# Performance work log

Measured on AMD Instinct MI355X. Metric: run time of the kernel, lower is better.

The kernel has to match this reference:

```python
import jax, jax.numpy as jnp
import numpy as np

EPS = 1e-5

def _conv3x3(x, w):
    # x: [n,c,h,w], w: [o,c,3,3], stride 1, padding 1 (SAME)
    return jax.lax.conv_general_dilated(x, w, (1, 1), 'SAME',
                                        dimension_numbers=('NCHW', 'OIHW', 'NCHW'))

def _bn(x, g, b, m, v):
    # inference-mode BatchNorm2d with running stats
    s = g / jnp.sqrt(v + EPS)
    return x * s[:, None, None] + (b - m * s)[:, None, None]

def _lrelu(x):
    return jnp.where(x > 0, x, 0.2 * x)

def _conv1x1(x, w, b):
    # w: [o,c] (1x1 conv kernel collapsed)
    return jnp.einsum('nchw,oc->nohw', x, w) + b[:, None, None]

def _conv_relu(x, w, g, b, m, v):
    return _lrelu(_bn(_conv3x3(x, w), g, b, m, v))

def _pam(f, Wq, bq, Wk, bk, Wv, bv, alpha):
    n, c, h, w = f.shape
    hw = h * w
    q = _conv1x1(f, Wq, bq).reshape(n, -1, hw)   # [n,cr,hw]
    k = _conv1x1(f, Wk, bk).reshape(n, -1, hw)   # [n,cr,hw]
    # attention[i,j] over spatial tokens, softmax along j
    attn = jax.nn.softmax(jnp.einsum('nci,ncj->nij', q, k), axis=-1)  # [n,hw,hw]
    v = _conv1x1(f, Wv, bv).reshape(n, c, hw)    # [n,c,hw]
    # torch: bmm(v, attn^T) -> out[:, :, i] = sum_j v[:, :, j] * attn[i, j]
    out = jnp.einsum('ncj,nij->nci', v, attn).reshape(n, c, h, w)
    return alpha * out + f

def _cam(f, W1, b1, W2, b2):
    s = jnp.mean(f, axis=(2, 3), keepdims=True)  # AdaptiveAvgPool2d(1)
    s = _lrelu(_conv1x1(s, W1, b1))
    s = jax.nn.sigmoid(_conv1x1(s, W2, b2))
    return f * s

def _upx2(x):
    n, c, h, w = x.shape
    return jax.image.resize(x, (n, c, 2 * h, 2 * w), 'bilinear')

def setup_inputs() -> dict:
    key = jax.random.key(0)
    ks = jax.random.split(key, 16)
    N, C, H, W_ = 4, 512, 64, 64
    CR, NC = C // 8, 64
    f32 = jnp.float32
    def nrm(k, shape, s=0.05):
        return jax.random.normal(k, shape, f32) * s
    return {
        'x': jax.random.normal(ks[0], (N, C, H, W_), f32),
        'W_pam_in': nrm(ks[1], (C, C, 3, 3)),
        'pam_gamma': jnp.ones((C,), f32), 'pam_beta': jnp.zeros((C,), f32),
        'pam_mean': nrm(ks[2], (C,)), 'pam_var': jax.random.uniform(ks[3], (C,), f32) + 0.5,
        'Wq': nrm(ks[4], (CR, C)), 'bq': jnp.zeros((CR,), f32),
        'Wk': nrm(ks[5], (CR, C)), 'bk': jnp.zeros((CR,), f32),
        'Wv': nrm(ks[6], (C, C)), 'bv': jnp.zeros((C,), f32),
        'alpha': nrm(ks[7], (1,), 1.0),
        'W_pam_out': nrm(ks[8], (NC, C)), 'b_pam_out': jnp.zeros((NC,), f32),
        'W_cam_in': nrm(ks[9], (C, C, 3, 3)),
        'cam_gamma': jnp.ones((C,), f32), 'cam_beta': jnp.zeros((C,), f32),
        'cam_mean': nrm(ks[10], (C,)), 'cam_var': jax.random.uniform(ks[11], (C,), f32) + 0.5,
        'Wc1': nrm(ks[12], (CR, C)), 'bc1': jnp.zeros((CR,), f32),
        'Wc2': nrm(ks[13], (C, CR)), 'bc2': jnp.zeros((C,), f32),
        'W_cam_out': nrm(ks[14], (NC, C)), 'b_cam_out': jnp.zeros((NC,), f32),
    }

def reference(x, W_pam_in, pam_gamma, pam_beta, pam_mean, pam_var,
              Wq, bq, Wk, bk, Wv, bv, alpha, W_pam_out, b_pam_out,
              W_cam_in, cam_gamma, cam_beta, cam_mean, cam_var,
              Wc1, bc1, Wc2, bc2, W_cam_out, b_cam_out):
    pam_feat = _conv_relu(x, W_pam_in, pam_gamma, pam_beta, pam_mean, pam_var)
    pam_feat = _pam(pam_feat, Wq, bq, Wk, bk, Wv, bv, alpha)
    pam_feat = _upx2(_conv1x1(pam_feat, W_pam_out, b_pam_out))
    cam_feat = _conv_relu(x, W_cam_in, cam_gamma, cam_beta, cam_mean, cam_var)
    cam_feat = _cam(cam_feat, Wc1, bc1, Wc2, bc2)
    cam_feat = _upx2(_conv1x1(cam_feat, W_cam_out, b_cam_out))
    return pam_feat + cam_feat
```

## Files before the change

### kernel.cpp

```cpp
#include <hip/hip_runtime.h>
#include <hip/hip_bf16.h>
#include <math.h>

#define N_  4
#define C_  512
#define H_  64
#define W_  64
#define HW_ 4096
#define CR_ 64
#define NC_ 64
#define EPSV 1e-5f

typedef __attribute__((ext_vector_type(8))) __bf16 bf16x8;
typedef __attribute__((ext_vector_type(4))) float f32x4;
typedef __hip_bfloat16 bf16s;

__device__ __forceinline__ unsigned short bfb(float f) {
    union { bf16s h; unsigned short u; } cv;
    cv.h = __float2bfloat16(f);
    return cv.u;
}

__device__ __forceinline__ float b2f(unsigned short h) {
    union { unsigned u; float f; } c; c.u = ((unsigned)h) << 16; return c.f;
}

__device__ __forceinline__ int swz8(int row, int ch) {
    return row * 64 + ((ch ^ (row & 7)) << 3);
}

__global__ __launch_bounds__(256) void k_xpose(
    const float* __restrict__ x, bf16s* __restrict__ xbT)
{
    __shared__ float xs[64][65];
    const int tid = threadIdx.x;
    const int n = blockIdx.z, c0 = blockIdx.y * 64, p0 = blockIdx.x * 64;
    for (int e = tid; e < 4096; e += 256) {
        int ci = e >> 6, pi = e & 63;
        xs[ci][pi] = x[((size_t)(n*C_ + c0 + ci))*HW_ + p0 + pi];
    }
    __syncthreads();
    for (int e = tid; e < 4096; e += 256) {
        int pi = e >> 6, ci = e & 63;
        xbT[((size_t)n*HW_ + p0 + pi)*C_ + c0 + ci] = __float2bfloat16(xs[ci][pi]);
    }
}

__global__ __launch_bounds__(256) void k_wprep(
    const float* __restrict__ w, bf16s* __restrict__ wb)
{
    int e = blockIdx.x * 256 + threadIdx.x;
    int c = e & 511; int r = e >> 9;
    int tap = r % 9; int o = r / 9;
    wb[e] = __float2bfloat16(w[((size_t)o*C_ + c)*9 + tap]);
}

__global__ __launch_bounds__(256) void k_wcast(
    const float* __restrict__ in, bf16s* __restrict__ out, int nElem)
{
    int e = blockIdx.x * 256 + threadIdx.x;
    if (e < nElem) out[e] = __float2bfloat16(in[e]);
}

__global__ __launch_bounds__(256, 3) void k_conv3x3_mfma(
    const bf16s* __restrict__ xbT,
    const bf16s* __restrict__ wb,  const bf16s* __restrict__ wb2,
    const float* __restrict__ gamma,  const float* __restrict__ beta,
    const float* __restrict__ mean,   const float* __restrict__ var,
    const float* __restrict__ gamma2, const float* __restrict__ beta2,
    const float* __restrict__ mean2,  const float* __restrict__ var2,
    bf16s* __restrict__ featT, bf16s* __restrict__ featT2,
    float* __restrict__ csum)
{
    __shared__ bf16s aL[3][128][36];
    __shared__ bf16s bL[132][36];
    const int tid = threadIdx.x;
    const int lid = blockIdx.x + (blockIdx.y << 5) + (blockIdx.z << 8);
    const int xcd = lid & 7;
    const int half = xcd >> 2;
    const int n    = xcd & 3;
    const int w8   = lid >> 3;
    const int o0 = (w8 >> 5) * 128;
    const int pt = w8 & 31;
    const int y0 = pt * 2;
    const bf16s* wbs = half ? wb2 : wb;
    const float* gm = half ? gamma2 : gamma;
    const float* bt = half ? beta2  : beta;
    const float* mn = half ? mean2  : mean;
    const float* vr = half ? var2   : var;
    bf16s* ft = half ? featT2 : featT;
    const int lane = tid & 63;
    const int wid  = tid >> 6;
    const int wr = wid >> 1, wc = wid & 1;
    const int lr = lane & 15, cb = lane >> 4;

    const int ao  = tid >> 2;
    const int ac  = (tid & 3) * 8;
    const int t0  = tid >> 2;
    const int t1  = t0 + 64;
    const int t2  = t0 + 128;
    const int ry1 = t1 >= 66 ? 1 : 0;
    const int xi1 = t1 - (ry1 ? 66 : 0);

    f32x4 acc[4][4];
#pragma unroll
    for (int i = 0; i < 4; ++i)
#pragma unroll
        for (int j = 0; j < 4; ++j) acc[i][j] = (f32x4){0.f,0.f,0.f,0.f};

    int4 pA0, pA1, pA2, pA3, pA4, pA5, pB0, pB1, pB2;

#define CONV_AADDR(DXI, OHALF, C0, DYI) \
    (const int4*)(wbs + ((size_t)(o0 + (OHALF) + ao)*9 + (DYI)*3 + (DXI))*C_ + (C0) + ac)

#define CONV_BLOAD(DST, RY, XI, C0, DYI, VALID)                               \
    {                                                                         \
        int row_ = y0 + (DYI) - 1 + (RY);                                     \
        int xc_  = (XI) - 1;                                                  \
        int4 v_ = {0,0,0,0};                                                  \
        if ((VALID) && row_ >= 0 && row_ < H_ && xc_ >= 0 && xc_ < W_)        \
            v_ = *(const int4*)(xbT +                                         \
                ((size_t)n*HW_ + row_*W_ + xc_)*C_ + (C0) + ac);              \
        DST = v_;                                                             \
    }

#define CONV_ISSUE(C0, DYI)                                                   \
    {                                                                         \
        pA0 = *CONV_AADDR(0,  0, C0, DYI);                                    \
        pA1 = *CONV_AADDR(0, 64, C0, DYI);                                    \
        pA2 = *CONV_AADDR(1,  0, C0, DYI);                                    \
        pA3 = *CONV_AADDR(1, 64, C0, DYI);                                    \
        pA4 = *CONV_AADDR(2,  0, C0, DYI);                                    \
        pA5 = *CONV_AADDR(2, 64, C0, DYI);                                    \
        CONV_BLOAD(pB0, 0, t0, C0, DYI, 1)                                    \
        CONV_BLOAD(pB1, ry1, xi1, C0, DYI, 1)                                 \
        CONV_BLOAD(pB2, 1, t2 - 66, C0, DYI, tid < 16)                        \
    }

    CONV_ISSUE(0, 0)
    int c0 = 0, dyi = 0;
    for (int it = 0; it < 48; ++it) {
        *(int4*)&aL[0][ao][ac]      = pA0;
        *(int4*)&aL[0][64 + ao][ac] = pA1;
        *(int4*)&aL[1][ao][ac]      = pA2;
        *(int4*)&aL[1][64 + ao][ac] = pA3;
        *(int4*)&aL[2][ao][ac]      = pA4;
        *(int4*)&aL[2][64 + ao][ac] = pA5;
        *(int4*)&bL[t0][ac] = pB0;
        *(int4*)&bL[t1][ac] = pB1;
        if (tid < 16) *(int4*)&bL[t2][ac] = pB2;
        __syncthreads();
        int nd = dyi + 1, nc = c0;
        if (nd == 3) { nd = 0; nc += 32; }
        if (it < 47) CONV_ISSUE(nc, nd)
#pragma unroll
        for (int dxi = 0; dxi < 3; ++dxi) {
            bf16x8 af[4], bfv[4];
#pragma unroll
            for (int fm = 0; fm < 4; ++fm)
                af[fm] = *(const bf16x8*)&aL[dxi][wr*64 + fm*16 + lr][cb*8];
#pragma unroll
            for (int fn = 0; fn < 4; ++fn) {
                int pg = wc*64 + fn*16 + lr;
                int ry = pg >> 6, xc = pg & 63;
                bfv[fn] = *(const bf16x8*)&bL[ry*66 + xc + dxi][cb*8];
            }
#pragma unroll
            for (int fm = 0; fm < 4; ++fm)
#pragma unroll
                for (int fn = 0; fn < 4; ++fn)
                    acc[fm][fn] = __builtin_amdgcn_mfma_f32_16x16x32_bf16(
                        af[fm], bfv[fn], acc[fm][fn], 0, 0, 0);
        }
        __syncthreads();
        c0 = nc; dyi = nd;
    }
#undef CONV_ISSUE
#undef CONV_BLOAD
#undef CONV_AADDR
#pragma unroll
    for (int fm = 0; fm < 4; ++fm) {
        float sc[4], sh[4];
        const int obase = o0 + wr*64 + fm*16 + cb*4;
#pragma unroll
        for (int r = 0; r < 4; ++r) {
            int o = obase + r;
            sc[r] = gm[o] * rsqrtf(vr[o] + EPSV);
            sh[r] = bt[o] - mn[o]*sc[r];
        }
        float ps[4] = {0.f, 0.f, 0.f, 0.f};
#pragma unroll
        for (int fn = 0; fn < 4; ++fn) {
            int pg = wc*64 + fn*16 + lr;
            int p  = pt*128 + pg;
            float vv[4];
#pragma unroll
            for (int r = 0; r < 4; ++r) {
                float t = fmaf(acc[fm][fn][r], sc[r], sh[r]);
                vv[r] = t > 0.f ? t : 0.2f*t;
                ps[r] += vv[r];
            }
            uint2 u;
            u.x = (unsigned)bfb(vv[0]) | ((unsigned)bfb(vv[1]) << 16);
            u.y = (unsigned)bfb(vv[2]) | ((unsigned)bfb(vv[3]) << 16);
            *(uint2*)&ft[((size_t)n*HW_ + p)*C_ + obase] = u;
        }
        if (half) {
#pragma unroll
            for (int r = 0; r < 4; ++r) {
                float s = ps[r];
                s += __shfl_xor(s, 1);
                s += __shfl_xor(s, 2);
                s += __shfl_xor(s, 4);
                s += __shfl_xor(s, 8);
                if (lr == 0) atomicAdd(&csum[n*C_ + obase + r], s);
            }
        }
    }
}

__global__ __launch_bounds__(256, 2) void k_gemm_qkv(
    const bf16s* __restrict__ Wqk, const bf16s* __restrict__ Wv,
    const bf16s* __restrict__ Bt,
    const float* __restrict__ bq, const float* __restrict__ bk,
    const float* __restrict__ bv,
    bf16s* __restrict__ qkb, bf16s* __restrict__ vb)
{
    __shared__ bf16s aL[64][36];
    __shared__ bf16s bL[256][36];
    const int tid = threadIdx.x;
    const int flat = blockIdx.x + (blockIdx.y << 4) + blockIdx.z * 160;
    const int k8 = flat & 7;
    const int n  = k8 >> 1;
    const int xh = k8 & 1;
    const int w8 = flat >> 3;
    const int yy = w8 % 10;
    const int p0 = ((((w8 / 10) << 1) | xh)) << 8;
    const bool isqk = (yy < 2);
    const int o0 = isqk ? yy*64 : (yy - 2)*64;
    const bf16s* A = isqk ? Wqk : Wv;
    const int lane = tid & 63;
    const int wid  = tid >> 6;
    const int lr = lane & 15, cb = lane >> 4;
    const int arow = tid >> 2, ach = (tid & 3) * 8;

    f32x4 acc[4][4];
#pragma unroll
    for (int i = 0; i < 4; ++i)
#pragma unroll
        for (int j = 0; j < 4; ++j) acc[i][j] = (f32x4){0.f,0.f,0.f,0.f};

    int4 pA, pB0, pB1, pB2, pB3;

#define GEMM_ISSUE(C0)                                                        \
    {                                                                         \
        pA = *(const int4*)&A[(size_t)(o0 + arow)*C_ + (C0) + ach];           \
        pB0 = *(const int4*)&Bt[((size_t)n*HW_ + p0 + arow      )*C_ + (C0) + ach]; \
        pB1 = *(const int4*)&Bt[((size_t)n*HW_ + p0 + arow +  64)*C_ + (C0) + ach]; \
        pB2 = *(const int4*)&Bt[((size_t)n*HW_ + p0 + arow + 128)*C_ + (C0) + ach]; \
        pB3 = *(const int4*)&Bt[((size_t)n*HW_ + p0 + arow + 192)*C_ + (C0) + ach]; \
    }

    GEMM_ISSUE(0)
    for (int c0 = 0; c0 < C_; c0 += 32) {
        *(int4*)&aL[arow][ach] = pA;
        *(int4*)&bL[arow      ][ach] = pB0;
        *(int4*)&bL[arow +  64][ach] = pB1;
        *(int4*)&bL[arow + 128][ach] = pB2;
        *(int4*)&bL[arow + 192][ach] = pB3;
        __syncthreads();
        if (c0 + 32 < C_) GEMM_ISSUE(c0 + 32)
        bf16x8 af[4], bfv[4];
#pragma unroll
        for (int fo = 0; fo < 4; ++fo)
            af[fo] = *(const bf16x8*)&aL[fo*16 + lr][cb*8];
#pragma unroll
        for (int fp = 0; fp < 4; ++fp)
            bfv[fp] = *(const bf16x8*)&bL[wid*64 + fp*16 + lr][cb*8];
#pragma unroll
        for (int fo = 0; fo < 4; ++fo)
#pragma unroll
            for (int fp = 0; fp < 4; ++fp)
                acc[fo][fp] = __builtin_amdgcn_mfma_f32_16x16x32_bf16(
                    af[fo], bfv[fp], acc[fo][fp], 0, 0, 0);
        __syncthreads();
    }
#undef GEMM_ISSUE
#pragma unroll
    for (int fo = 0; fo < 4; ++fo) {
        const int obase = o0 + fo*16 + cb*4;
        const float* bp = isqk ? ((obase >> 6) ? bk : bq) : bv;
        const int bofs = isqk ? (obase & 63) : obase;
        float bv4[4];
#pragma unroll
        for (int r = 0; r < 4; ++r) bv4[r] = bp[bofs + r];
#pragma unroll
        for (int fp = 0; fp < 4; ++fp) {
            int p = p0 + wid*64 + fp*16 + lr;
            float v[4];
#pragma unroll
            for (int r = 0; r < 4; ++r) v[r] = acc[fo][fp][r] + bv4[r];
            if (isqk) {
                uint2 u;
                u.x = (unsigned)bfb(v[0]) | ((unsigned)bfb(v[1]) << 16);
                u.y = (unsigned)bfb(v[2]) | ((unsigned)bfb(v[3]) << 16);
                size_t base = (((size_t)((obase >> 6) * N_ + n))*HW_ + p)*64
                              + (obase & 63);
                *(uint2*)&qkb[base] = u;
            } else {
#pragma unroll
                for (int r = 0; r < 4; ++r)
                    vb[((size_t)(n*C_ + obase + r))*HW_ + p] =
                        __float2bfloat16(v[r]);
            }
        }
    }
}

__global__ __launch_bounds__(256, 2) void k_gemm(
    const bf16s* __restrict__ A, const bf16s* __restrict__ Bt,
    const float* __restrict__ bias, const float* __restrict__ scale,
    float* __restrict__ outp, int O)
{
    __shared__ bf16s aL[64][36];
    __shared__ bf16s bL[256][36];
    const int tid = threadIdx.x;
    const int n  = blockIdx.z;
    const int p0 = blockIdx.x * 256;
    const int o0 = blockIdx.y * 64;
    const int lane = tid & 63;
    const int wid  = tid >> 6;
    const int lr = lane & 15, cb = lane >> 4;
    const int arow = tid >> 2, ach = (tid & 3) * 8;

    f32x4 acc[4][4];
#pragma unroll
    for (int i = 0; i < 4; ++i)
#pragma unroll
        for (int j = 0; j < 4; ++j) acc[i][j] = (f32x4){0.f,0.f,0.f,0.f};

    int4 pA, pB0, pB1, pB2, pB3;
    float4 pS0, pS1;

#define GEMM_ISSUE(C0)                                                        \
    {                                                                         \
        pA = *(const int4*)&A[(size_t)(o0 + arow)*C_ + (C0) + ach];           \
        if (scale) {                                                          \
            pS0 = *(const float4*)&scale[(size_t)n*C_ + (C0) + ach];          \
            pS1 = *(const float4*)&scale[(size_t)n*C_ + (C0) + ach + 4];      \
        }                                                                     \
        pB0 = *(const int4*)&Bt[((size_t)n*HW_ + p0 + arow      )*C_ + (C0) + ach]; \
        pB1 = *(const int4*)&Bt[((size_t)n*HW_ + p0 + arow +  64)*C_ + (C0) + ach]; \
        pB2 = *(const int4*)&Bt[((size_t)n*HW_ + p0 + arow + 128)*C_ + (C0) + ach]; \
        pB3 = *(const int4*)&Bt[((size_t)n*HW_ + p0 + arow + 192)*C_ + (C0) + ach]; \
    }

    GEMM_ISSUE(0)
    for (int c0 = 0; c0 < C_; c0 += 32) {
        if (scale) {
            const bf16s* sp = (const bf16s*)&pA;
            bf16s tmp[8];
            tmp[0] = __float2bfloat16(__bfloat162float(sp[0]) * pS0.x);
            tmp[1] = __float2bfloat16(__bfloat162float(sp[1]) * pS0.y);
            tmp[2] = __float2bfloat16(__bfloat162float(sp[2]) * pS0.z);
            tmp[3] = __float2bfloat16(__bfloat162float(sp[3]) * pS0.w);
            tmp[4] = __float2bfloat16(__bfloat162float(sp[4]) * pS1.x);
            tmp[5] = __float2bfloat16(__bfloat162float(sp[5]) * pS1.y);
            tmp[6] = __float2bfloat16(__bfloat162float(sp[6]) * pS1.z);
            tmp[7] = __float2bfloat16(__bfloat162float(sp[7]) * pS1.w);
            *(int4*)&aL[arow][ach] = *(int4*)tmp;
        } else {
            *(int4*)&aL[arow][ach] = pA;
        }
        *(int4*)&bL[arow      ][ach] = pB0;
        *(int4*)&bL[arow +  64][ach] = pB1;
        *(int4*)&bL[arow + 128][ach] = pB2;
        *(int4*)&bL[arow + 192][ach] = pB3;
        __syncthreads();
        if (c0 + 32 < C_) GEMM_ISSUE(c0 + 32)
        bf16x8 af[4], bfv[4];
#pragma unroll
        for (int fo = 0; fo < 4; ++fo)
            af[fo] = *(const bf16x8*)&aL[fo*16 + lr][cb*8];
#pragma unroll
        for (int fp = 0; fp < 4; ++fp)
            bfv[fp] = *(const bf16x8*)&bL[wid*64 + fp*16 + lr][cb*8];
#pragma unroll
        for (int fo = 0; fo < 4; ++fo)
#pragma unroll
            for (int fp = 0; fp < 4; ++fp)
                acc[fo][fp] = __builtin_amdgcn_mfma_f32_16x16x32_bf16(
                    af[fo], bfv[fp], acc[fo][fp], 0, 0, 0);
        __syncthreads();
    }
#undef GEMM_ISSUE
#pragma unroll
    for (int fo = 0; fo < 4; ++fo) {
        const int obase = o0 + fo*16 + cb*4;
        float bv[4];
#pragma unroll
        for (int r = 0; r < 4; ++r) bv[r] = bias[obase + r];
#pragma unroll
        for (int fp = 0; fp < 4; ++fp) {
            int p = p0 + wid*64 + fp*16 + lr;
#pragma unroll
            for (int r = 0; r < 4; ++r)
                outp[((size_t)(n*O + obase + r))*HW_ + p] =
                    acc[fo][fp][r] + bv[r];
        }
    }
}

__global__ __launch_bounds__(256) void k_rowstats_mfma(
    const bf16s* __restrict__ qb, const bf16s* __restrict__ kb,
    float* __restrict__ rowm, float* __restrict__ rowl)
{
    __shared__ bf16s qs[4096];
    __shared__ bf16s ks[2][4096];
    const int tid = threadIdx.x;
    const int lid = blockIdx.x + (blockIdx.y << 6) + (blockIdx.z << 8);
    const int n  = lid & 3;
    const int jz = (lid >> 2) & 1;
    const int i0 = (lid >> 3) << 6;
    const int lane = tid & 63;
    const int wid  = tid >> 6;
    const int lr = lane & 15, cb = lane >> 4;

    for (int e = tid; e < 512; e += 256) {
        int row = e >> 3, ch = e & 7;
        *(int4*)&qs[swz8(row, ch)] =
            *(const int4*)&qb[((size_t)n*HW_ + i0 + row)*CR_ + ch*8];
    }
    const int krow = tid >> 3, kch = tid & 7;
    const bf16s* kbase = kb + (size_t)n*HW_*CR_ + (size_t)jz*2048*CR_ + kch*8;
    int4 kreg0 = *(const int4*)(kbase + (size_t)krow*CR_);
    int4 kreg1 = *(const int4*)(kbase + (size_t)(krow + 32)*CR_);
    *(int4*)&ks[0][swz8(krow, kch)] = kreg0;
    *(int4*)&ks[0][swz8(krow + 32, kch)] = kreg1;
    kreg0 = *(const int4*)(kbase + (size_t)(64 + krow)*CR_);
    kreg1 = *(const int4*)(kbase + (size_t)(64 + krow + 32)*CR_);
    __syncthreads();
    bf16x8 bq[2];
#pragma unroll
    for (int kk = 0; kk < 2; ++kk)
        bq[kk] = *(const bf16x8*)&qs[swz8(wid*16 + lr, kk*4 + cb)];

    float m_t = -INFINITY, l_t = 0.f;
    for (int t = 0; t < 32; ++t) {
        const bf16s* kst = ks[t & 1];
        f32x4 sv[4];
#pragma unroll
        for (int fj = 0; fj < 4; ++fj) {
            f32x4 s = (f32x4){0.f,0.f,0.f,0.f};
#pragma unroll
            for (int kk = 0; kk < 2; ++kk) {
                bf16x8 ak = *(const bf16x8*)&kst[swz8(fj*16 + lr, kk*4 + cb)];
                s = __builtin_amdgcn_mfma_f32_16x16x32_bf16(ak, bq[kk], s, 0, 0, 0);
            }
            sv[fj] = s;
        }
        if (t < 31) {
            *(int4*)&ks[(t + 1) & 1][swz8(krow, kch)] = kreg0;
            *(int4*)&ks[(t + 1) & 1][swz8(krow + 32, kch)] = kreg1;
            if (t < 30) {
                kreg0 = *(const int4*)(kbase + (size_t)((t+2)*64 + krow)*CR_);
                kreg1 = *(const int4*)(kbase + (size_t)((t+2)*64 + krow + 32)*CR_);
            }
        }
        float mx = m_t;
#pragma unroll
        for (int fj = 0; fj < 4; ++fj)
#pragma unroll
            for (int r = 0; r < 4; ++r) mx = fmaxf(mx, sv[fj][r]);
        float sum = 0.f;
#pragma unroll
        for (int fj = 0; fj < 4; ++fj)
#pragma unroll
            for (int r = 0; r < 4; ++r) sum += __expf(sv[fj][r] - mx);
        l_t = l_t * __expf(m_t - mx) + sum;
        m_t = mx;
        __syncthreads();
    }
#pragma unroll
    for (int mask = 16; mask <= 32; mask <<= 1) {
        float mo = __shfl_xor(m_t, mask);
        float lo = __shfl_xor(l_t, mask);
        float m2 = fmaxf(m_t, mo);
        l_t = l_t * __expf(m_t - m2) + lo * __expf(mo - m2);
        m_t = m2;
    }
    if (cb == 0) {
        rowm[((size_t)jz*N_ + n)*HW_ + i0 + wid*16 + lr] = m_t;
        rowl[((size_t)jz*N_ + n)*HW_ + i0 + wid*16 + lr] = l_t;
    }
}

__global__ __launch_bounds__(256, 4) void k_pv_mfma(
    const bf16s* __restrict__ qb, const bf16s* __restrict__ kb,
    const bf16s* __restrict__ vb, const float* __restrict__ rowm,
    const float* __restrict__ rowl, const float* __restrict__ alpha,
    bf16s* __restrict__ featT)
{
    __shared__ bf16s ks[2][4096];
    __shared__ bf16s ps[2][4096];
    const int tid = threadIdx.x;
    const int lid = blockIdx.x + (blockIdx.y << 6) + (blockIdx.z << 8);
    const int k8  = lid & 7;
    const int n   = k8 >> 1;
    const int cc0 = (((lid >> 3) & 1) * 2 + (k8 & 1)) << 7;
    const int i0  = (lid >> 4) << 6;
    const int lane = tid & 63;
    const int wid  = tid >> 6;
    const int lr = lane & 15, cb = lane >> 4;

    for (int e = tid; e < 512; e += 256) {
        int row = e >> 3, ch = e & 7;
        *(int4*)&ks[0][swz8(row, ch)] =
            *(const int4*)&qb[((size_t)n*HW_ + i0 + row)*CR_ + ch*8];
    }
    const int krow = tid >> 3, kch = tid & 7;
    const bf16s* kbase = kb + (size_t)n*HW_*CR_ + kch*8;
    int4 kreg0 = *(const int4*)(kbase + (size_t)krow*CR_);
    int4 kreg1 = *(const int4*)(kbase + (size_t)(krow + 32)*CR_);
    __syncthreads();
    bf16x8 bq[2];
#pragma unroll
    for (int kk = 0; kk < 2; ++kk)
        bq[kk] = *(const bf16x8*)&ks[0][swz8(wid*16 + lr, kk*4 + cb)];

    const size_t sidx = (size_t)n*HW_ + i0 + wid*16 + lr;
    const float m0 = rowm[sidx], m1 = rowm[sidx + (size_t)N_*HW_];
    const float l0 = rowl[sidx], l1 = rowl[sidx + (size_t)N_*HW_];
    const float mreg = fmaxf(m0, m1);
    const float rinv = 1.f / (l0*__expf(m0 - mreg) + l1*__expf(m1 - mreg));
    const float al = alpha[0];
    __syncthreads();
    *(int4*)&ks[0][swz8(krow, kch)] = kreg0;
    *(int4*)&ks[0][swz8(krow + 32, kch)] = kreg1;
    kreg0 = *(const int4*)(kbase + (size_t)(64 + krow)*CR_);
    kreg1 = *(const int4*)(kbase + (size_t)(64 + krow + 32)*CR_);
    __syncthreads();

    f32x4 acc[2][4];
#pragma unroll
    for (int i = 0; i < 2; ++i)
#pragma unroll
        for (int j = 0; j < 4; ++j) acc[i][j] = (f32x4){0.f,0.f,0.f,0.f};

    const bf16s* vbase = vb + ((size_t)(n*C_ + cc0 + wid*32))*HW_;
    bf16x8 vc0, vc1, vc2, vc3, vn0, vn1, vn2, vn3;

    for (int jt = 0; jt < 64; ++jt) {
        const bf16s* vj = vbase + jt*64;
        vn0 = *(const bf16x8*)(vj + (size_t)(     lr)*HW_      + cb*8);
        vn1 = *(const bf16x8*)(vj + (size_t)(16 + lr)*HW_      + cb*8);
        vn2 = *(const bf16x8*)(vj + (size_t)(     lr)*HW_ + 32 + cb*8);
        vn3 = *(const bf16x8*)(vj + (size_t)(16 + lr)*HW_ + 32 + cb*8);
        if (jt > 0) {
            const bf16s* pp = ps[(jt - 1) & 1];
            bf16x8 pa[4];
#pragma unroll
            for (int fi = 0; fi < 4; ++fi)
                pa[fi] = *(const bf16x8*)&pp[swz8(fi*16 + lr, cb)];
#pragma unroll
            for (int fi = 0; fi < 4; ++fi) {
                acc[0][fi] = __builtin_amdgcn_mfma_f32_16x16x32_bf16(
                    vc0, pa[fi], acc[0][fi], 0, 0, 0);
                acc[1][fi] = __builtin_amdgcn_mfma_f32_16x16x32_bf16(
                    vc1, pa[fi], acc[1][fi], 0, 0, 0);
            }
#pragma unroll
            for (int fi = 0; fi < 4; ++fi)
                pa[fi] = *(const bf16x8*)&pp[swz8(fi*16 + lr, 4 + cb)];
#pragma unroll
            for (int fi = 0; fi < 4; ++fi) {
                acc[0][fi] = __builtin_amdgcn_mfma_f32_16x16x32_bf16(
                    vc2, pa[fi], acc[0][fi], 0, 0, 0);
                acc[1][fi] = __builtin_amdgcn_mfma_f32_16x16x32_bf16(
                    vc3, pa[fi], acc[1][fi], 0, 0, 0);
            }
        }
        {
            const bf16s* kst = ks[jt & 1];
            bf16s* pst = ps[jt & 1];
#pragma unroll
            for (int fj = 0; fj < 4; ++fj) {
                f32x4 s = (f32x4){0.f,0.f,0.f,0.f};
#pragma unroll
                for (int kk = 0; kk < 2; ++kk) {
                    bf16x8 ak = *(const bf16x8*)&kst[swz8(fj*16 + lr, kk*4 + cb)];
                    s = __builtin_amdgcn_mfma_f32_16x16x32_bf16(ak, bq[kk], s, 0, 0, 0);
                }
                unsigned short b[4];
#pragma unroll
                for (int r = 0; r < 4; ++r)
                    b[r] = bfb(__expf(s[r] - mreg) * rinv);
                uint2 u;
                u.x = (unsigned)b[0] | ((unsigned)b[1] << 16);
                u.y = (unsigned)b[2] | ((unsigned)b[3] << 16);
                *(uint2*)&pst[swz8(wid*16 + lr, fj*2 + (cb >> 1)) + (cb & 1)*4] = u;
            }
        }
        if (jt < 63) {
            *(int4*)&ks[(jt + 1) & 1][swz8(krow, kch)] = kreg0;
            *(int4*)&ks[(jt + 1) & 1][swz8(krow + 32, kch)] = kreg1;
            if (jt < 62) {
                kreg0 = *(const int4*)(kbase + (size_t)((jt+2)*64 + krow)*CR_);
                kreg1 = *(const int4*)(kbase + (size_t)((jt+2)*64 + krow + 32)*CR_);
            }
        }
        vc0 = vn0; vc1 = vn1; vc2 = vn2; vc3 = vn3;
        __syncthreads();
    }
    {
        const bf16s* pp = ps[63 & 1];
        bf16x8 pa[4];
#pragma unroll
        for (int fi = 0; fi < 4; ++fi)
            pa[fi] = *(const bf16x8*)&pp[swz8(fi*16 + lr, cb)];
#pragma unroll
        for (int fi = 0; fi < 4; ++fi) {
            acc[0][fi] = __builtin_amdgcn_mfma_f32_16x16x32_bf16(
                vc0, pa[fi], acc[0][fi], 0, 0, 0);
            acc[1][fi] = __builtin_amdgcn_mfma_f32_16x16x32_bf16(
                vc1, pa[fi], acc[1][fi], 0, 0, 0);
        }
#pragma unroll
        for (int fi = 0; fi < 4; ++fi)
            pa[fi] = *(const bf16x8*)&pp[swz8(fi*16 + lr, 4 + cb)];
#pragma unroll
        for (int fi = 0; fi < 4; ++fi) {
            acc[0][fi] = __builtin_amdgcn_mfma_f32_16x16x32_bf16(
                vc2, pa[fi], acc[0][fi], 0, 0, 0);
            acc[1][fi] = __builtin_amdgcn_mfma_f32_16x16x32_bf16(
                vc3, pa[fi], acc[1][fi], 0, 0, 0);
        }
    }
#pragma unroll
    for (int fc2 = 0; fc2 < 2; ++fc2) {
        const int ccl = wid*32 + fc2*16 + cb*4;
#pragma unroll
        for (int fi = 0; fi < 4; ++fi) {
            const int p = i0 + fi*16 + lr;
            bf16s* fb = &featT[((size_t)n*HW_ + p)*C_ + cc0 + ccl];
            uint2 fv = *(const uint2*)fb;
            float f0 = b2f((unsigned short)(fv.x & 0xffff));
            float f1 = b2f((unsigned short)(fv.x >> 16));
            float f2 = b2f((unsigned short)(fv.y & 0xffff));
            float f3 = b2f((unsigned short)(fv.y >> 16));
            float v0 = fmaf(al, acc[fc2][fi][0], f0);
            float v1 = fmaf(al, acc[fc2][fi][1], f1);
            float v2 = fmaf(al, acc[fc2][fi][2], f2);
            float v3 = fmaf(al, acc[fc2][fi][3], f3);
            uint2 u;
            u.x = (unsigned)bfb(v0) | ((unsigned)bfb(v1) << 16);
            u.y = (unsigned)bfb(v2) | ((unsigned)bfb(v3) << 16);
            *(uint2*)fb = u;
        }
    }
}

__global__ __launch_bounds__(64) void k_cmlp(
    const float* __restrict__ s0, const float* __restrict__ Wc1,
    const float* __restrict__ bc1, const float* __restrict__ Wc2,
    const float* __restrict__ bc2, float* __restrict__ s2)
{
    const int n = blockIdx.x, tid = threadIdx.x;
    __shared__ float s1s[64];
    float a = 0.f;
    for (int c = 0; c < C_; ++c)
        a = fmaf(Wc1[(size_t)tid*C_ + c], s0[n*C_ + c] * (1.f/HW_), a);
    a += bc1[tid];
    a = a > 0.f ? a : 0.2f*a;
    s1s[tid] = a;
    __syncthreads();
    for (int c = tid; c < C_; c += 64) {
        float b = 0.f;
        for (int i = 0; i < CR_; ++i) b = fmaf(Wc2[(size_t)c*CR_ + i], s1s[i], b);
        b += bc2[c];
        s2[n*C_ + c] = 1.f / (1.f + __expf(-b));
    }
}

__global__ __launch_bounds__(256) void k_up(
    const float* __restrict__ pl, const float* __restrict__ cl,
    float* __restrict__ out)
{
    int idx = blockIdx.x * 256 + threadIdx.x;
    int ox = idx & 127; int rest = idx >> 7;
    int oy = rest & 127; rest >>= 7;
    int o  = rest & 63;  int n = rest >> 6;
    float fy = oy*0.5f - 0.25f;
    float fx = ox*0.5f - 0.25f;
    int y0 = (int)floorf(fy); float wy = fy - y0;
    int x0 = (int)floorf(fx); float wx = fx - x0;
    int y0c = y0 < 0 ? 0 : y0;      int y1c = y0+1 > 63 ? 63 : y0+1;
    int x0c = x0 < 0 ? 0 : x0;      int x1c = x0+1 > 63 ? 63 : x0+1;
    const float* a = pl + ((size_t)(n*NC_ + o))*HW_;
    const float* b = cl + ((size_t)(n*NC_ + o))*HW_;
    float v00 = a[y0c*64+x0c] + b[y0c*64+x0c];
    float v01 = a[y0c*64+x1c] + b[y0c*64+x1c];
    float v10 = a[y1c*64+x0c] + b[y1c*64+x0c];
    float v11 = a[y1c*64+x1c] + b[y1c*64+x1c];
    out[idx] = (1.f-wy)*((1.f-wx)*v00 + wx*v01) + wy*((1.f-wx)*v10 + wx*v11);
}

extern "C" void kernel_launch(void* const* d_in, const int* in_sizes, int n_in,
                              void* d_out, int out_size, void* d_ws, size_t ws_size,
                              hipStream_t stream)
{
    const float* x         = (const float*)d_in[0];
    const float* W_pam_in  = (const float*)d_in[1];
    const float* pam_g     = (const float*)d_in[2];
    const float* pam_b     = (const float*)d_in[3];
    const float* pam_m     = (const float*)d_in[4];
    const float* pam_v     = (const float*)d_in[5];
    const float* Wq        = (const float*)d_in[6];
    const float* bq        = (const float*)d_in[7];
    const float* Wk        = (const float*)d_in[8];
    const float* bk        = (const float*)d_in[9];
    const float* Wv        = (const float*)d_in[10];
    const float* bv        = (const float*)d_in[11];
    const float* alpha     = (const float*)d_in[12];
    const float* W_pam_out = (const float*)d_in[13];
    const float* b_pam_out = (const float*)d_in[14];
    const float* W_cam_in  = (const float*)d_in[15];
    const float* cam_g     = (const float*)d_in[16];
    const float* cam_b     = (const float*)d_in[17];
    const float* cam_m     = (const float*)d_in[18];
    const float* cam_v     = (const float*)d_in[19];
    const float* Wc1       = (const float*)d_in[20];
    const float* bc1       = (const float*)d_in[21];
    const float* Wc2       = (const float*)d_in[22];
    const float* bc2       = (const float*)d_in[23];
    const float* W_cam_out = (const float*)d_in[24];
    const float* b_cam_out = (const float*)d_in[25];

    float* pam_low = (float*)d_ws;
    float* rowm    = pam_low + 1048576;
    float* rowl    = rowm    + 32768;
    float* s0      = rowl    + 32768;
    float* s2      = s0      + 2048;
    bf16s* xbT     = (bf16s*)(s2 + 2048);
    bf16s* featTb  = xbT + 8388608;
    bf16s* featTb2 = featTb + 8388608;
    bf16s* vb      = featTb2 + 8388608;
    bf16s* qb      = vb + 8388608;
    bf16s* kb      = qb + 1048576;
    bf16s* wbp     = kb + 1048576;
    bf16s* wbp2    = wbp + 2359296;
    bf16s* Wqb     = wbp2 + 2359296;
    bf16s* Wkb     = Wqb + 32768;
    bf16s* Wvb     = Wkb + 32768;
    bf16s* Wpob    = Wvb + 262144;
    bf16s* Wcob    = Wpob + 32768;
    float* cam_low = (float*)qb;

    dim3 b256(256);
    k_xpose<<<dim3(64,8,4), b256, 0, stream>>>(x, xbT);
    k_wcast<<<dim3(128), b256, 0, stream>>>(Wq, Wqb, 32768);
    k_wcast<<<dim3(128), b256, 0, stream>>>(Wk, Wkb, 32768);
    k_wcast<<<dim3(1024), b256, 0, stream>>>(Wv, Wvb, 262144);
    k_wcast<<<dim3(128), b256, 0, stream>>>(W_pam_out, Wpob, 32768);
    k_wcast<<<dim3(128), b256, 0, stream>>>(W_cam_out, Wcob, 32768);
    hipMemsetAsync(s0, 0, 2048*sizeof(float), stream);
    k_wprep<<<dim3(9216), b256, 0, stream>>>(W_pam_in, wbp);
    k_wprep<<<dim3(9216), b256, 0, stream>>>(W_cam_in, wbp2);
    k_conv3x3_mfma<<<dim3(32,8,4), b256, 0, stream>>>(
        xbT, wbp, wbp2, pam_g, pam_b, pam_m, pam_v,
        cam_g, cam_b, cam_m, cam_v, featTb, featTb2, s0);
    k_gemm_qkv<<<dim3(16,10,4), b256, 0, stream>>>(
        Wqb, Wvb, featTb, bq, bk, bv, qb, vb);
    k_rowstats_mfma<<<dim3(64,4,2), b256, 0, stream>>>(qb, kb, rowm, rowl);
    k_pv_mfma<<<dim3(64,4,4), b256, 0, stream>>>(
        qb, kb, vb, rowm, rowl, alpha, featTb);
    k_gemm<<<dim3(16,1,4), b256, 0, stream>>>(
        Wpob, featTb, b_pam_out, nullptr, pam_low, 64);
    k_cmlp<<<dim3(4), dim3(64), 0, stream>>>(s0, Wc1, bc1, Wc2, bc2, s2);
    k_gemm<<<dim3(16,1,4), b256, 0, stream>>>(
        Wcob, featTb2, b_cam_out, s2, cam_low, 64);
    k_up<<<dim3(16384), b256, 0, stream>>>(pam_low, cam_low, (float*)d_out);
}
```

Baseline: 451.8 us.

## Double-buffer conv3x3 LDS tiles and merge the two output GEMMs into one launch

```diff
diff --git a/kernel.cpp b/kernel.cpp
--- a/kernel.cpp
+++ b/kernel.cpp
@@ -62,7 +62,7 @@
     if (e < nElem) out[e] = __float2bfloat16(in[e]);
 }
 
-__global__ __launch_bounds__(256, 3) void k_conv3x3_mfma(
+__global__ __launch_bounds__(256, 2) void k_conv3x3_mfma(
     const bf16s* __restrict__ xbT,
     const bf16s* __restrict__ wb,  const bf16s* __restrict__ wb2,
     const float* __restrict__ gamma,  const float* __restrict__ beta,
@@ -72,8 +72,8 @@
     bf16s* __restrict__ featT, bf16s* __restrict__ featT2,
     float* __restrict__ csum)
 {
-    __shared__ bf16s aL[3][128][36];
-    __shared__ bf16s bL[132][36];
+    __shared__ bf16s aL[2][3][128][36];
+    __shared__ bf16s bL[2][132][36];
     const int tid = threadIdx.x;
     const int lid = blockIdx.x + (blockIdx.y << 5) + (blockIdx.z << 8);
     const int xcd = lid & 7;
@@ -137,33 +137,45 @@
         CONV_BLOAD(pB2, 1, t2 - 66, C0, DYI, tid < 16)                        \
     }
 
+#define CONV_COMMIT(B)                                                        \
+    {                                                                         \
+        *(int4*)&aL[B][0][ao][ac]      = pA0;                                 \
+        *(int4*)&aL[B][0][64 + ao][ac] = pA1;                                 \
+        *(int4*)&aL[B][1][ao][ac]      = pA2;                                 \
+        *(int4*)&aL[B][1][64 + ao][ac] = pA3;                                 \
+        *(int4*)&aL[B][2][ao][ac]      = pA4;                                 \
+        *(int4*)&aL[B][2][64 + ao][ac] = pA5;                                 \
+        *(int4*)&bL[B][t0][ac] = pB0;                                         \
+        *(int4*)&bL[B][t1][ac] = pB1;                                         \
+        if (tid < 16) *(int4*)&bL[B][t2][ac] = pB2;                           \
+    }
+
+    int nc = 0, nd = 0;
     CONV_ISSUE(0, 0)
-    int c0 = 0, dyi = 0;
+    CONV_COMMIT(0)
+    nd = 1;
+    CONV_ISSUE(nc, nd)
+    __syncthreads();
     for (int it = 0; it < 48; ++it) {
-        *(int4*)&aL[0][ao][ac]      = pA0;
-        *(int4*)&aL[0][64 + ao][ac] = pA1;
-        *(int4*)&aL[1][ao][ac]      = pA2;
-        *(int4*)&aL[1][64 + ao][ac] = pA3;
-        *(int4*)&aL[2][ao][ac]      = pA4;
-        *(int4*)&aL[2][64 + ao][ac] = pA5;
-        *(int4*)&bL[t0][ac] = pB0;
-        *(int4*)&bL[t1][ac] = pB1;
-        if (tid < 16) *(int4*)&bL[t2][ac] = pB2;
-        __syncthreads();
-        int nd = dyi + 1, nc = c0;
-        if (nd == 3) { nd = 0; nc += 32; }
-        if (it < 47) CONV_ISSUE(nc, nd)
+        const int buf = it & 1;
+        if (it < 47) {
+            CONV_COMMIT(buf ^ 1)
+            if (it < 46) {
+                nd = nd + 1; if (nd == 3) { nd = 0; nc += 32; }
+                CONV_ISSUE(nc, nd)
+            }
+        }
 #pragma unroll
         for (int dxi = 0; dxi < 3; ++dxi) {
             bf16x8 af[4], bfv[4];
 #pragma unroll
             for (int fm = 0; fm < 4; ++fm)
-                af[fm] = *(const bf16x8*)&aL[dxi][wr*64 + fm*16 + lr][cb*8];
+                af[fm] = *(const bf16x8*)&aL[buf][dxi][wr*64 + fm*16 + lr][cb*8];
 #pragma unroll
             for (int fn = 0; fn < 4; ++fn) {
                 int pg = wc*64 + fn*16 + lr;
                 int ry = pg >> 6, xc = pg & 63;
-                bfv[fn] = *(const bf16x8*)&bL[ry*66 + xc + dxi][cb*8];
+                bfv[fn] = *(const bf16x8*)&bL[buf][ry*66 + xc + dxi][cb*8];
             }
 #pragma unroll
             for (int fm = 0; fm < 4; ++fm)
@@ -173,8 +185,8 @@
                         af[fm], bfv[fn], acc[fm][fn], 0, 0, 0);
         }
         __syncthreads();
-        c0 = nc; dyi = nd;
-    }
+    }
+#undef CONV_COMMIT
 #undef CONV_ISSUE
 #undef CONV_BLOAD
 #undef CONV_AADDR
@@ -317,17 +329,24 @@
     }
 }
 
-__global__ __launch_bounds__(256, 2) void k_gemm(
-    const bf16s* __restrict__ A, const bf16s* __restrict__ Bt,
-    const float* __restrict__ bias, const float* __restrict__ scale,
-    float* __restrict__ outp, int O)
+__global__ __launch_bounds__(256, 2) void k_gemm_tail(
+    const bf16s* __restrict__ Wpob, const bf16s* __restrict__ Wcob,
+    const bf16s* __restrict__ featT, const bf16s* __restrict__ featT2,
+    const float* __restrict__ b_pam, const float* __restrict__ b_cam,
+    const float* __restrict__ s2,
+    float* __restrict__ pam_low, float* __restrict__ cam_low)
 {
     __shared__ bf16s aL[64][36];
     __shared__ bf16s bL[256][36];
     const int tid = threadIdx.x;
+    const int half = blockIdx.y;
     const int n  = blockIdx.z;
     const int p0 = blockIdx.x * 256;
-    const int o0 = blockIdx.y * 64;
+    const bf16s* A = half ? Wcob : Wpob;
+    const bf16s* Bt = half ? featT2 : featT;
+    const float* bias = half ? b_cam : b_pam;
+    const float* scale = half ? s2 : nullptr;
+    float* outp = half ? cam_low : pam_low;
     const int lane = tid & 63;
     const int wid  = tid >> 6;
     const int lr = lane & 15, cb = lane >> 4;
@@ -344,7 +363,7 @@
 
 #define GEMM_ISSUE(C0)                                                        \
     {                                                                         \
-        pA = *(const int4*)&A[(size_t)(o0 + arow)*C_ + (C0) + ach];           \
+        pA = *(const int4*)&A[(size_t)arow*C_ + (C0) + ach];                  \
         if (scale) {                                                          \
             pS0 = *(const float4*)&scale[(size_t)n*C_ + (C0) + ach];          \
             pS1 = *(const float4*)&scale[(size_t)n*C_ + (C0) + ach + 4];      \
@@ -396,7 +415,7 @@
 #undef GEMM_ISSUE
 #pragma unroll
     for (int fo = 0; fo < 4; ++fo) {
-        const int obase = o0 + fo*16 + cb*4;
+        const int obase = fo*16 + cb*4;
         float bv[4];
 #pragma unroll
         for (int r = 0; r < 4; ++r) bv[r] = bias[obase + r];
@@ -405,7 +424,7 @@
             int p = p0 + wid*64 + fp*16 + lr;
 #pragma unroll
             for (int r = 0; r < 4; ++r)
-                outp[((size_t)(n*O + obase + r))*HW_ + p] =
+                outp[((size_t)(n*NC_ + obase + r))*HW_ + p] =
                     acc[fo][fp][r] + bv[r];
         }
     }
@@ -772,12 +791,11 @@
     k_gemm_qkv<<<dim3(16,10,4), b256, 0, stream>>>(
         Wqb, Wvb, featTb, bq, bk, bv, qb, vb);
     k_rowstats_mfma<<<dim3(64,4,2), b256, 0, stream>>>(qb, kb, rowm, rowl);
+    k_cmlp<<<dim3(4), dim3(64), 0, stream>>>(s0, Wc1, bc1, Wc2, bc2, s2);
     k_pv_mfma<<<dim3(64,4,4), b256, 0, stream>>>(
         qb, kb, vb, rowm, rowl, alpha, featTb);
-    k_gemm<<<dim3(16,1,4), b256, 0, stream>>>(
-        Wpob, featTb, b_pam_out, nullptr, pam_low, 64);
-    k_cmlp<<<dim3(4), dim3(64), 0, stream>>>(s0, Wc1, bc1, Wc2, bc2, s2);
-    k_gemm<<<dim3(16,1,4), b256, 0, stream>>>(
-        Wcob, featTb2, b_cam_out, s2, cam_low, 64);
+    k_gemm_tail<<<dim3(16,2,4), b256, 0, stream>>>(
+        Wpob, Wcob, featTb, featTb2, b_pam_out, b_cam_out, s2,
+        pam_low, cam_low);
     k_up<<<dim3(16384), b256, 0, stream>>>(pam_low, cam_low, (float*)d_out);
 }
```

Result: no change. 445.0 us (-1.5%).
